# Kernel tuning notes

Hardware: AMD Instinct MI355X
Metric: run time of the kernel (lower is better)

The kernel has to match this reference:

```python
import jax, jax.numpy as jnp
import numpy as np

B, N, IN_DIM, HID, K = 32, 512, 1024, 512, 3
ALPHA = 0.2  # leaky_relu negative slope
NEG = -9e15


def setup_inputs() -> dict:
    key = jax.random.key(0)
    ks = jax.random.split(key, 7)
    hidden_states = jax.random.normal(ks[0], (B, N, IN_DIM), jnp.float32)
    adj = (jax.random.uniform(ks[1], (B, 3, N, N)) < 0.05).astype(jnp.float32)
    W_all = jax.random.normal(ks[2], (3, K, IN_DIM, HID), jnp.float32) * 0.02
    a_all = jax.random.normal(ks[3], (3, K, 2 * HID, 1), jnp.float32) * 0.02
    wawa_w = jax.random.normal(ks[4], (HID, 100), jnp.float32) * 0.05
    wawa_b = jnp.zeros((100,), jnp.float32)
    ctx_w = jax.random.normal(ks[5], (100, 1), jnp.float32) * 0.05
    return {"hidden_states": hidden_states, "adj": adj, "W_all": W_all,
            "a_all": a_all, "wawa_w": wawa_w, "wawa_b": wawa_b, "ctx_w": ctx_w}


def _gat(adj_m, x, W, a):
    # e_ij = leaky_relu(cat[h_i, h_j] @ a) == leaky_relu(h_i@a1 + h_j@a2)
    h = jnp.einsum('bnf,fh->bnh', x, W)           # [B,N,HID]
    f1 = jnp.einsum('bnh,ho->bno', h, a[:HID])    # [B,N,1]
    f2 = jnp.einsum('bnh,ho->bno', h, a[HID:])    # [B,N,1]
    e = jax.nn.leaky_relu(f1 + jnp.swapaxes(f2, 1, 2), negative_slope=ALPHA)  # [B,N,N]
    att = jnp.where(adj_m > 0, e, NEG)
    att = jax.nn.softmax(att, axis=2)
    return jnp.einsum('bnm,bmh->bnh', att, h)


def reference(hidden_states, adj, W_all, a_all, wawa_w, wawa_b, ctx_w):
    adj_a, adj_b, adj_c = adj[:, 0], adj[:, 1], adj[:, 2]
    pa, pb, pc = adj_a, adj_b, adj_c  # matmuls(A, k) = A^(k+1)
    hs = []
    for layer in range(K):
        if layer > 0:
            pa = jnp.matmul(pa, adj_a)
            pb = jnp.matmul(pb, adj_b)
            pc = jnp.matmul(pc, adj_c)
        h_layer = (_gat(pa, hidden_states, W_all[0, layer], a_all[0, layer])
                   + _gat(pb, hidden_states, W_all[1, layer], a_all[1, layer])
                   + _gat(pc, hidden_states, W_all[2, layer], a_all[2, layer]))
        hs.append(h_layer)
    # attention-based combination over the K orders
    s = [jnp.einsum('bnc,co->bno', jnp.tanh(jnp.einsum('bnh,hc->bnc', h, wawa_w) + wawa_b), ctx_w)
         for h in hs]                              # each [B,N,1]
    vs = jax.nn.softmax(jnp.concatenate(s, axis=2), axis=2)  # [B,N,K]
    h_stack = jnp.stack(hs, axis=2)                # [B,N,K,HID]
    return jnp.sum(vs[..., None] * h_stack, axis=2)  # [B,N,HID]
```

## Files before the change

kernel.cpp:

```cpp
#include <hip/hip_runtime.h>
#include <hip/hip_bf16.h>

typedef short v8s __attribute__((ext_vector_type(8)));
typedef float v4f __attribute__((ext_vector_type(4)));
typedef unsigned long long u64;

#define ALPHA 0.2f

__device__ inline unsigned short f32_bf16(float x){
    unsigned int u = __float_as_uint(x);
    unsigned int r = (u + 0x7fffu + ((u >> 16) & 1u)) >> 16;
    return (unsigned short)r;
}
__device__ inline float bf16_f32(unsigned short s){
    return __uint_as_float(((unsigned int)s) << 16);
}
__device__ inline v4f mfma16(v8s a, v8s b, v4f c){
    return __builtin_amdgcn_mfma_f32_16x16x32_bf16(a, b, c, 0, 0, 0);
}
__device__ inline void gload16(const unsigned short* g, short* l){
    __builtin_amdgcn_global_load_lds((const __attribute__((address_space(1))) unsigned int*)g,
                                     (__attribute__((address_space(3))) unsigned int*)l,
                                     16, 0, 0);
}


__global__ void k_convert_x(const float* __restrict__ x, v8s* __restrict__ out, int n8){
    int i = blockIdx.x * 256 + threadIdx.x;
    if (i >= n8) return;
    const float4* p = (const float4*)x + (size_t)i * 2;
    float4 a = p[0], b = p[1];
    v8s r;
    r[0] = (short)f32_bf16(a.x); r[1] = (short)f32_bf16(a.y);
    r[2] = (short)f32_bf16(a.z); r[3] = (short)f32_bf16(a.w);
    r[4] = (short)f32_bf16(b.x); r[5] = (short)f32_bf16(b.y);
    r[6] = (short)f32_bf16(b.z); r[7] = (short)f32_bf16(b.w);
    out[i] = r;
}

__global__ void k_transpose_w(const float* __restrict__ W, unsigned short* __restrict__ Wt){
    __shared__ float tile[32][33];
    int g = blockIdx.z, k0 = blockIdx.x * 32, h0 = blockIdx.y * 32;
    int tx = threadIdx.x, ty = threadIdx.y;
    #pragma unroll
    for (int i = 0; i < 4; ++i)
        tile[ty + i*8][tx] = W[((size_t)g*1024 + k0 + ty + i*8)*512 + h0 + tx];
    __syncthreads();
    #pragma unroll
    for (int i = 0; i < 4; ++i){
        int h = ty + i*8;
        Wt[((size_t)g*512 + h0 + h)*1024 + k0 + tx] = f32_bf16(tile[tx][h]);
    }
}

__global__ void k_wawat(const float* __restrict__ w, unsigned short* __restrict__ wt){
    int i = blockIdx.x * 256 + threadIdx.x;
    if (i >= 128 * 512) return;
    int c = i >> 9, k = i & 511;
    wt[i] = (c < 100) ? f32_bf16(w[k*100 + c]) : (unsigned short)0;
}


__global__ void k_bits(const float* __restrict__ adj, u64* __restrict__ bits){
    int row = blockIdx.x;
    int t = row >> 14, b = (row >> 9) & 31, i = row & 511;
    const float* src = adj + (((size_t)b*3 + t)*512 + i)*512;
    int lane = threadIdx.x;
    #pragma unroll
    for (int w = 0; w < 8; ++w){
        u64 word = __ballot(src[w*64 + lane] > 0.5f);
        if (lane == 0) bits[(size_t)row*8 + w] = word;
    }
}

__global__ __launch_bounds__(256) void k_boolmm(const u64* __restrict__ prev,
                                                const u64* __restrict__ base,
                                                u64* __restrict__ out){
    int row = blockIdx.x * 256 + threadIdx.x;
    if (row >= 49152) return;
    int tb = row >> 9;
    const u64* pr = prev + (size_t)row * 8;
    const u64* bb = base + ((size_t)tb << 9) * 8;
    ulonglong2 a0 = {0,0}, a1 = {0,0}, a2 = {0,0}, a3 = {0,0};
    #pragma unroll
    for (int w = 0; w < 8; ++w){
        u64 m = pr[w];
        const u64* bw = bb + (size_t)(w << 6) * 8;
        while (m){
            int k = __builtin_ctzll(m);
            m &= m - 1;
            const ulonglong2* br = (const ulonglong2*)(bw + (size_t)k * 8);
            ulonglong2 b0 = br[0], b1 = br[1], b2 = br[2], b3 = br[3];
            a0.x |= b0.x; a0.y |= b0.y;
            a1.x |= b1.x; a1.y |= b1.y;
            a2.x |= b2.x; a2.y |= b2.y;
            a3.x |= b3.x; a3.y |= b3.y;
        }
    }
    ulonglong2* op = (ulonglong2*)(out + (size_t)row * 8);
    op[0] = a0; op[1] = a1; op[2] = a2; op[3] = a3;
}

__global__ __launch_bounds__(256, 4) void k_gemm_h(
    const unsigned short* __restrict__ Wt, const unsigned short* __restrict__ Xb,
    unsigned short* __restrict__ Ht, int l)
{
    __shared__ __align__(16) short As[128*32];
    __shared__ __align__(16) short Bs[128*32];
    const int bn = blockIdx.x, bm = blockIdx.y, t = blockIdx.z;
    const int g = t*3 + l;
    const int tid = threadIdx.x;
    const int lane = tid & 63, wave = tid >> 6;
    const int wr = wave >> 1, wc = wave & 1;
    const int fr = lane & 15, fq = lane >> 4;
    const int slot = fq ^ (fr & 3) ^ ((fr >> 2) & 3);

    const int srow = tid >> 2, sw = tid & 3;
    const int gw = sw ^ (srow & 3) ^ ((srow >> 2) & 3);
    const unsigned short* Ap = Wt + ((size_t)g*512 + (size_t)bm*128 + srow)*1024 + gw*8;
    const unsigned short* Bp = Xb + ((size_t)bn*128 + srow)*1024 + gw*8;
    short* AsW = As + wave*512;
    short* BsW = Bs + wave*512;

    v4f acc[4][4] = {};

    for (int kt = 0; kt < 32; ++kt){
        const unsigned short* a0 = Ap + kt*32;
        const unsigned short* b0 = Bp + kt*32;
        gload16(a0,           AsW);
        gload16(a0 + 64*1024, AsW + 2048);
        gload16(b0,           BsW);
        gload16(b0 + 64*1024, BsW + 2048);
        __syncthreads();
        v8s af[4], bf[4];
        #pragma unroll
        for (int i = 0; i < 4; ++i) af[i] = *(const v8s*)&As[(wr*64 + i*16 + fr)*32 + slot*8];
        #pragma unroll
        for (int i = 0; i < 4; ++i) bf[i] = *(const v8s*)&Bs[(wc*64 + i*16 + fr)*32 + slot*8];
        #pragma unroll
        for (int i = 0; i < 4; ++i)
            #pragma unroll
            for (int j = 0; j < 4; ++j)
                acc[i][j] = mfma16(af[i], bf[j], acc[i][j]);
        __syncthreads();
    }
    #pragma unroll
    for (int i = 0; i < 4; ++i){
        const int h = bm*128 + wr*64 + i*16 + fq*4;
        #pragma unroll
        for (int j = 0; j < 4; ++j){
            const int mc = bn*128 + wc*64 + j*16 + fr;
            unsigned short* dst = Ht + ((size_t)t*512 + h)*16384 + mc;
            #pragma unroll
            for (int rg = 0; rg < 4; ++rg)
                dst[(size_t)rg*16384] = f32_bf16(acc[i][j][rg]);
        }
    }
}

__global__ __launch_bounds__(256) void k_f1f2(
    const unsigned short* __restrict__ Ht, const float* __restrict__ aall,
    float* __restrict__ f1, float* __restrict__ f2, int l)
{
    __shared__ float red[256][4];
    const int t = blockIdx.y;
    const int ml = threadIdx.x & 63, hq = threadIdx.x >> 6;
    const int m = (blockIdx.x * 64 + ml) * 2;
    const float* a1 = aall + ((size_t)t*3 + l)*1024;
    const float* a2 = a1 + 512;
    const unsigned int* hp = (const unsigned int*)(Ht + (size_t)t*512*16384 + m);
    float s1a = 0.f, s1b = 0.f, s2a = 0.f, s2b = 0.f;
    #pragma unroll 4
    for (int hh = 0; hh < 128; ++hh){
        int h = hq*128 + hh;
        unsigned int pv = hp[(size_t)h*8192];
        float va = bf16_f32((unsigned short)(pv & 0xffffu));
        float vb = bf16_f32((unsigned short)(pv >> 16));
        float c1 = a1[h], c2 = a2[h];
        s1a += va*c1; s2a += va*c2;
        s1b += vb*c1; s2b += vb*c2;
    }
    red[threadIdx.x][0] = s1a; red[threadIdx.x][1] = s1b;
    red[threadIdx.x][2] = s2a; red[threadIdx.x][3] = s2b;
    __syncthreads();
    if (hq == 0){
        #pragma unroll
        for (int j = 1; j < 4; ++j){
            s1a += red[ml + 64*j][0]; s1b += red[ml + 64*j][1];
            s2a += red[ml + 64*j][2]; s2b += red[ml + 64*j][3];
        }
        f1[t*16384 + m]     = s1a;
        f1[t*16384 + m + 1] = s1b;
        f2[t*16384 + m]     = s2a;
        f2[t*16384 + m + 1] = s2b;
    }
}

__device__ inline void softmax_row(int t, int b, int rt, int r, int q,
    const float* __restrict__ f1a, const float* __restrict__ f2a,
    const u64* __restrict__ maskP, float* p)
{
    const float f1v = f1a[t*16384 + b*512 + rt*64 + r];
    const u64 mw = maskP[(((size_t)t*32 + b)*512 + rt*64 + r)*8 + q];
    const float4* f2p = (const float4*)(f2a + t*16384 + b*512 + q*64);
    float sm = 0.f;
    #pragma unroll
    for (int w = 0; w < 16; ++w){
        float4 f4 = f2p[w];
        #pragma unroll
        for (int u2 = 0; u2 < 4; ++u2){
            int u = w*4 + u2;
            float e = f1v + ((const float*)&f4)[u2];
            e = (e >= 0.f) ? e : ALPHA*e;
            float pe = ((mw >> u) & 1ull) ? __expf(e) : 0.f;
            p[u] = pe; sm += pe;
        }
    }
    sm += __shfl_xor(sm, 1);
    sm += __shfl_xor(sm, 2);
    sm += __shfl_xor(sm, 4);
    const float rinv = 1.f / (sm + 1e-30f);
    #pragma unroll
    for (int u = 0; u < 64; ++u) p[u] *= rinv;
}

__device__ inline void store_att(short* __restrict__ attbuf, int r, int q,
                                 const float* p)
{
    #pragma unroll
    for (int j8 = 0; j8 < 8; ++j8){
        v8s pk;
        #pragma unroll
        for (int u = 0; u < 8; ++u) pk[u] = (short)f32_bf16(p[j8*8 + u]);
        const int cs = q*8 + (j8 ^ q);
        *(v8s*)&attbuf[r*520 + cs*8] = pk;
    }
}

__device__ inline void pv_accum(const short* __restrict__ attbuf,
    const unsigned short* __restrict__ Hb, int wave, int fr, int fq, v4f acc[4][4])
{
    #pragma unroll 2
    for (int kk = 0; kk < 16; ++kk){
        v8s af[4], bv[4];
        const int cb = kk*4 + fq;
        const int cs = (cb & 56) | ((cb & 7) ^ ((cb >> 3) & 7));
        #pragma unroll
        for (int i = 0; i < 4; ++i)
            af[i] = *(const v8s*)&attbuf[(i*16 + fr)*520 + cs*8];
        #pragma unroll
        for (int j = 0; j < 4; ++j)
            bv[j] = *(const v8s*)(Hb + (size_t)(wave*64 + j*16 + fr)*16384 + kk*32 + fq*8);
        #pragma unroll
        for (int i = 0; i < 4; ++i)
            #pragma unroll
            for (int j = 0; j < 4; ++j)
                acc[i][j] = mfma16(af[i], bv[j], acc[i][j]);
    }
}

__global__ __launch_bounds__(512, 2) void k_att_pv(
    const unsigned short* __restrict__ Ht,
    const float* __restrict__ f1a, const float* __restrict__ f2a,
    const u64* __restrict__ maskP,
    unsigned short* __restrict__ hlb)
{
    __shared__ __align__(16) short att0[64*520];
    __shared__ __align__(16) short att1[64*520];
    const int tid = threadIdx.x;
    const int lane = tid & 63, wave = tid >> 6;
    const int b = blockIdx.x, rt = blockIdx.y;
    const int r = tid >> 3, q = tid & 7;
    const int fr = lane & 15, fq = lane >> 4;
    v4f acc[4][4] = {};
    float p[64];

    const unsigned short* Hb0 = Ht + (size_t)b*512;

    softmax_row(0, b, rt, r, q, f1a, f2a, maskP, p);
    store_att(att0, r, q, p);
    __syncthreads();

    softmax_row(1, b, rt, r, q, f1a, f2a, maskP, p);
    store_att(att1, r, q, p);
    pv_accum(att0, Hb0, wave, fr, fq, acc);
    __syncthreads();

    softmax_row(2, b, rt, r, q, f1a, f2a, maskP, p);
    store_att(att0, r, q, p);
    pv_accum(att1, Hb0 + (size_t)512*16384, wave, fr, fq, acc);
    __syncthreads();

    pv_accum(att0, Hb0 + (size_t)2*512*16384, wave, fr, fq, acc);

    #pragma unroll
    for (int i = 0; i < 4; ++i){
        const int row = rt*64 + i*16 + fq*4;
        #pragma unroll
        for (int j = 0; j < 4; ++j){
            const int col = wave*64 + j*16 + fr;
            unsigned short* d1 = hlb + ((size_t)b*512 + row)*512 + col;
            #pragma unroll
            for (int rg = 0; rg < 4; ++rg)
                d1[(size_t)rg*512] = f32_bf16(acc[i][j][rg]);
        }
    }
}

__global__ __launch_bounds__(256) void k_gemm_s(
    const unsigned short* __restrict__ Hb, const unsigned short* __restrict__ Wwt,
    float* __restrict__ C1)
{
    __shared__ __align__(16) short As[128*32];
    __shared__ __align__(16) short Bs[128*32];
    const int bm = blockIdx.x;
    const int tid = threadIdx.x;
    const int lane = tid & 63, wave = tid >> 6;
    const int wr = wave >> 1, wc = wave & 1;
    const int fr = lane & 15, fq = lane >> 4;
    const int slot = fq ^ (fr & 3) ^ ((fr >> 2) & 3);
    const int srow = tid >> 2, sw = tid & 3;
    const int gw = sw ^ (srow & 3) ^ ((srow >> 2) & 3);
    const unsigned short* Ap = Hb + ((size_t)bm*128 + srow)*512 + gw*8;
    const unsigned short* Bp = Wwt + (size_t)srow*512 + gw*8;

    v4f acc[4][4] = {};
    v8s ra0 = *(const v8s*)(Ap);
    v8s ra1 = *(const v8s*)(Ap + 64*512);
    v8s rb0 = *(const v8s*)(Bp);
    v8s rb1 = *(const v8s*)(Bp + 64*512);

    for (int kt = 0; kt < 16; ++kt){
        __syncthreads();
        *(v8s*)&As[tid*8]        = ra0;
        *(v8s*)&As[tid*8 + 2048] = ra1;
        *(v8s*)&Bs[tid*8]        = rb0;
        *(v8s*)&Bs[tid*8 + 2048] = rb1;
        __syncthreads();
        if (kt + 1 < 16){
            const unsigned short* An = Ap + (kt+1)*32;
            const unsigned short* Bn = Bp + (kt+1)*32;
            ra0 = *(const v8s*)(An); ra1 = *(const v8s*)(An + 64*512);
            rb0 = *(const v8s*)(Bn); rb1 = *(const v8s*)(Bn + 64*512);
        }
        v8s af[4], bf[4];
        #pragma unroll
        for (int i = 0; i < 4; ++i) af[i] = *(const v8s*)&As[(wr*64 + i*16 + fr)*32 + slot*8];
        #pragma unroll
        for (int i = 0; i < 4; ++i) bf[i] = *(const v8s*)&Bs[(wc*64 + i*16 + fr)*32 + slot*8];
        #pragma unroll
        for (int i = 0; i < 4; ++i)
            #pragma unroll
            for (int j = 0; j < 4; ++j)
                acc[i][j] = mfma16(af[i], bf[j], acc[i][j]);
    }
    #pragma unroll
    for (int i = 0; i < 4; ++i)
        #pragma unroll
        for (int j = 0; j < 4; ++j)
            #pragma unroll
            for (int rg = 0; rg < 4; ++rg)
                C1[((size_t)bm*128 + wr*64 + i*16 + fq*4 + rg)*128 + wc*64 + j*16 + fr]
                    = acc[i][j][rg];
}

__global__ void k_sv(const float* __restrict__ C1, const float* __restrict__ wb,
                     const float* __restrict__ cw, float* __restrict__ v)
{
    int m = blockIdx.x * 256 + threadIdx.x;
    if (m >= 16384) return;
    float s[3];
    #pragma unroll
    for (int l = 0; l < 3; ++l){
        const float* row = C1 + ((size_t)l*16384 + m)*128;
        float a = 0.f;
        for (int c = 0; c < 100; ++c){
            float x = row[c] + wb[c];
            float th;
            if (x > 15.f) th = 1.f;
            else if (x < -15.f) th = -1.f;
            else { float ex = __expf(2.f*x); th = (ex - 1.f) / (ex + 1.f); }
            a += th * cw[c];
        }
        s[l] = a;
    }
    float m0 = fmaxf(s[0], fmaxf(s[1], s[2]));
    float e0 = __expf(s[0]-m0), e1 = __expf(s[1]-m0), e2 = __expf(s[2]-m0);
    float inv = 1.f / (e0 + e1 + e2);
    v[m] = e0*inv; v[16384 + m] = e1*inv; v[32768 + m] = e2*inv;
}

__global__ void k_comb(const unsigned short* __restrict__ hlb, const float* __restrict__ v,
                       float* __restrict__ out)
{
    int idx = blockIdx.x * 256 + threadIdx.x;
    if (idx >= 16384*64) return;
    int m = idx >> 6, c8 = (idx & 63) << 3;
    const unsigned short* hp = hlb + (size_t)m*512 + c8;
    v8s a = *(const v8s*)hp;
    v8s bb = *(const v8s*)(hp + (size_t)16384*512);
    v8s cc = *(const v8s*)(hp + (size_t)2*16384*512);
    float v0 = v[m], v1 = v[16384+m], v2 = v[32768+m];
    float o[8];
    #pragma unroll
    for (int u = 0; u < 8; ++u)
        o[u] = v0*bf16_f32((unsigned short)a[u])
             + v1*bf16_f32((unsigned short)bb[u])
             + v2*bf16_f32((unsigned short)cc[u]);
    float4* dst = (float4*)(out + (size_t)m*512 + c8);
    dst[0] = make_float4(o[0], o[1], o[2], o[3]);
    dst[1] = make_float4(o[4], o[5], o[6], o[7]);
}

extern "C" void kernel_launch(void* const* d_in, const int* in_sizes, int n_in,
                              void* d_out, int out_size, void* d_ws, size_t ws_size,
                              hipStream_t stream)
{
    (void)in_sizes; (void)n_in; (void)out_size; (void)ws_size;
    const float* hs   = (const float*)d_in[0];
    const float* adj  = (const float*)d_in[1];
    const float* W    = (const float*)d_in[2];
    const float* aall = (const float*)d_in[3];
    const float* ww   = (const float*)d_in[4];
    const float* wb   = (const float*)d_in[5];
    const float* cw   = (const float*)d_in[6];
    float* out = (float*)d_out;
    char* ws = (char*)d_ws;

    unsigned short* Xb  = (unsigned short*)(ws);
    unsigned short* Wt  = (unsigned short*)(ws + 33554432);
    unsigned short* Wwt = (unsigned short*)(ws + 42991616);
    u64* bits           = (u64*)(ws + 43122688);
    u64* P2             = (u64*)(ws + 46268416);
    u64* P3             = (u64*)(ws + 49414144);
    unsigned short* Ht  = (unsigned short*)(ws + 52559872);
    float* f1           = (float*)(ws + 102891520);
    float* f2           = (float*)(ws + 103088128);
    unsigned short* hlb = (unsigned short*)(ws + 203948032);
    float* C1           = (float*)(ws + 52559872);
    float* vv           = (float*)(ws + 102891520);

    k_convert_x<<<8192, 256, 0, stream>>>(hs, (v8s*)Xb, 2097152);
    k_transpose_w<<<dim3(32,16,9), dim3(32,8), 0, stream>>>(W, Wt);
    k_wawat<<<256, 256, 0, stream>>>(ww, Wwt);
    k_bits<<<49152, 64, 0, stream>>>(adj, bits);
    k_boolmm<<<192, 256, 0, stream>>>(bits, bits, P2);
    k_boolmm<<<192, 256, 0, stream>>>(bits, P2, P3);

    const u64* masks[3] = {bits, P2, P3};
    for (int l = 0; l < 3; ++l){
        k_gemm_h<<<dim3(128,4,3), 256, 0, stream>>>(Wt, Xb, Ht, l);
        k_f1f2<<<dim3(128,3), 256, 0, stream>>>(Ht, aall, f1, f2, l);
        k_att_pv<<<dim3(32,8), 512, 0, stream>>>(Ht, f1, f2, masks[l],
            hlb + (size_t)l*16384*512);
    }
    k_gemm_s<<<384, 256, 0, stream>>>(hlb, Wwt, C1);
    k_sv<<<64, 256, 0, stream>>>(C1, wb, cw, vv);
    k_comb<<<4096, 256, 0, stream>>>(hlb, vv, out);
}
```

Before: 624.9 us.

## Fuse f1/f2 projection into GEMM epilogue, batch bit-packing rows, prefetch PV operands

The f1/f2 attention projections are now computed from the fp32 accumulators in the k_gemm_h epilogue. Partial sums go through shuffles and shared memory, then a small k_f1red kernel adds the four bm partials. This removes the k_f1f2 kernel, which re-read the whole bf16 H tensor with strided loads. k_bits now packs four rows per 256-thread block instead of one row per 64-thread block, and pv_accum double-buffers the global H operand loads one k-step ahead. The fused epilogue takes the projection from fp32 accumulators rather than bf16-rounded H, which changes numerics slightly, and the prefetch adds register pressure.

```diff
diff --git a/kernel.cpp b/kernel.cpp
--- a/kernel.cpp
+++ b/kernel.cpp
@@ -61,11 +61,12 @@
 }
 
 
-__global__ void k_bits(const float* __restrict__ adj, u64* __restrict__ bits){
-    int row = blockIdx.x;
+__global__ __launch_bounds__(256) void k_bits(const float* __restrict__ adj,
+                                              u64* __restrict__ bits){
+    int row = blockIdx.x * 4 + (threadIdx.x >> 6);
     int t = row >> 14, b = (row >> 9) & 31, i = row & 511;
     const float* src = adj + (((size_t)b*3 + t)*512 + i)*512;
-    int lane = threadIdx.x;
+    int lane = threadIdx.x & 63;
     #pragma unroll
     for (int w = 0; w < 8; ++w){
         u64 word = __ballot(src[w*64 + lane] > 0.5f);
@@ -103,7 +104,8 @@
 
 __global__ __launch_bounds__(256, 4) void k_gemm_h(
     const unsigned short* __restrict__ Wt, const unsigned short* __restrict__ Xb,
-    unsigned short* __restrict__ Ht, int l)
+    unsigned short* __restrict__ Ht, const float* __restrict__ aall,
+    float* __restrict__ f1p, float* __restrict__ f2p, int l)
 {
     __shared__ __align__(16) short As[128*32];
     __shared__ __align__(16) short Bs[128*32];
@@ -156,44 +158,62 @@
                 dst[(size_t)rg*16384] = f32_bf16(acc[i][j][rg]);
         }
     }
-}
-
-__global__ __launch_bounds__(256) void k_f1f2(
-    const unsigned short* __restrict__ Ht, const float* __restrict__ aall,
-    float* __restrict__ f1, float* __restrict__ f2, int l)
-{
-    __shared__ float red[256][4];
-    const int t = blockIdx.y;
-    const int ml = threadIdx.x & 63, hq = threadIdx.x >> 6;
-    const int m = (blockIdx.x * 64 + ml) * 2;
     const float* a1 = aall + ((size_t)t*3 + l)*1024;
     const float* a2 = a1 + 512;
-    const unsigned int* hp = (const unsigned int*)(Ht + (size_t)t*512*16384 + m);
-    float s1a = 0.f, s1b = 0.f, s2a = 0.f, s2b = 0.f;
-    #pragma unroll 4
-    for (int hh = 0; hh < 128; ++hh){
-        int h = hq*128 + hh;
-        unsigned int pv = hp[(size_t)h*8192];
-        float va = bf16_f32((unsigned short)(pv & 0xffffu));
-        float vb = bf16_f32((unsigned short)(pv >> 16));
-        float c1 = a1[h], c2 = a2[h];
-        s1a += va*c1; s2a += va*c2;
-        s1b += vb*c1; s2b += vb*c2;
-    }
-    red[threadIdx.x][0] = s1a; red[threadIdx.x][1] = s1b;
-    red[threadIdx.x][2] = s2a; red[threadIdx.x][3] = s2b;
+    float s1[4] = {0.f,0.f,0.f,0.f}, s2[4] = {0.f,0.f,0.f,0.f};
+    #pragma unroll
+    for (int i = 0; i < 4; ++i){
+        #pragma unroll
+        for (int rg = 0; rg < 4; ++rg){
+            const int h = bm*128 + wr*64 + i*16 + fq*4 + rg;
+            const float c1 = a1[h], c2 = a2[h];
+            #pragma unroll
+            for (int j = 0; j < 4; ++j){
+                s1[j] += acc[i][j][rg]*c1;
+                s2[j] += acc[i][j][rg]*c2;
+            }
+        }
+    }
+    #pragma unroll
+    for (int j = 0; j < 4; ++j){
+        s1[j] += __shfl_xor(s1[j], 16); s1[j] += __shfl_xor(s1[j], 32);
+        s2[j] += __shfl_xor(s2[j], 16); s2[j] += __shfl_xor(s2[j], 32);
+    }
+    float* scr = (float*)As;
     __syncthreads();
-    if (hq == 0){
-        #pragma unroll
-        for (int j = 1; j < 4; ++j){
-            s1a += red[ml + 64*j][0]; s1b += red[ml + 64*j][1];
-            s2a += red[ml + 64*j][2]; s2b += red[ml + 64*j][3];
-        }
-        f1[t*16384 + m]     = s1a;
-        f1[t*16384 + m + 1] = s1b;
-        f2[t*16384 + m]     = s2a;
-        f2[t*16384 + m + 1] = s2b;
-    }
+    if (fq == 0){
+        #pragma unroll
+        for (int j = 0; j < 4; ++j){
+            scr[(((wr*2 + wc)*4 + j)*16 + fr)*2 + 0] = s1[j];
+            scr[(((wr*2 + wc)*4 + j)*16 + fr)*2 + 1] = s2[j];
+        }
+    }
+    __syncthreads();
+    if (tid < 256){
+        const int which = tid & 1, fr2 = (tid >> 1) & 15, j2 = (tid >> 5) & 3,
+                  wc2 = (tid >> 7) & 1;
+        const float v = scr[(((0*2 + wc2)*4 + j2)*16 + fr2)*2 + which]
+                      + scr[(((1*2 + wc2)*4 + j2)*16 + fr2)*2 + which];
+        const int m = bn*128 + wc2*64 + j2*16 + fr2;
+        float* dst = which ? f2p : f1p;
+        dst[((size_t)bm*3 + t)*16384 + m] = v;
+    }
+}
+
+__global__ __launch_bounds__(256) void k_f1red(
+    const float* __restrict__ f1p, const float* __restrict__ f2p,
+    float* __restrict__ f1, float* __restrict__ f2)
+{
+    int idx = blockIdx.x * 256 + threadIdx.x;
+    if (idx >= 49152) return;
+    float s1 = 0.f, s2 = 0.f;
+    #pragma unroll
+    for (int bm = 0; bm < 4; ++bm){
+        int t = idx >> 14, m = idx & 16383;
+        s1 += f1p[((size_t)bm*3 + t)*16384 + m];
+        s2 += f2p[((size_t)bm*3 + t)*16384 + m];
+    }
+    f1[idx] = s1; f2[idx] = s2;
 }
 
 __device__ inline void softmax_row(int t, int b, int rt, int r, int q,
@@ -240,22 +260,44 @@
 __device__ inline void pv_accum(const short* __restrict__ attbuf,
     const unsigned short* __restrict__ Hb, int wave, int fr, int fq, v4f acc[4][4])
 {
-    #pragma unroll 2
+    v8s bv0[4], bv1[4];
+    #pragma unroll
+    for (int j = 0; j < 4; ++j)
+        bv0[j] = *(const v8s*)(Hb + (size_t)(wave*64 + j*16 + fr)*16384 + fq*8);
+    #pragma unroll
     for (int kk = 0; kk < 16; ++kk){
-        v8s af[4], bv[4];
+        if (kk + 1 < 16){
+            if ((kk + 1) & 1){
+                #pragma unroll
+                for (int j = 0; j < 4; ++j)
+                    bv1[j] = *(const v8s*)(Hb + (size_t)(wave*64 + j*16 + fr)*16384
+                                           + (kk+1)*32 + fq*8);
+            } else {
+                #pragma unroll
+                for (int j = 0; j < 4; ++j)
+                    bv0[j] = *(const v8s*)(Hb + (size_t)(wave*64 + j*16 + fr)*16384
+                                           + (kk+1)*32 + fq*8);
+            }
+        }
+        v8s af[4];
         const int cb = kk*4 + fq;
         const int cs = (cb & 56) | ((cb & 7) ^ ((cb >> 3) & 7));
         #pragma unroll
         for (int i = 0; i < 4; ++i)
             af[i] = *(const v8s*)&attbuf[(i*16 + fr)*520 + cs*8];
-        #pragma unroll
-        for (int j = 0; j < 4; ++j)
-            bv[j] = *(const v8s*)(Hb + (size_t)(wave*64 + j*16 + fr)*16384 + kk*32 + fq*8);
-        #pragma unroll
-        for (int i = 0; i < 4; ++i)
-            #pragma unroll
-            for (int j = 0; j < 4; ++j)
-                acc[i][j] = mfma16(af[i], bv[j], acc[i][j]);
+        if (kk & 1){
+            #pragma unroll
+            for (int i = 0; i < 4; ++i)
+                #pragma unroll
+                for (int j = 0; j < 4; ++j)
+                    acc[i][j] = mfma16(af[i], bv1[j], acc[i][j]);
+        } else {
+            #pragma unroll
+            for (int i = 0; i < 4; ++i)
+                #pragma unroll
+                for (int j = 0; j < 4; ++j)
+                    acc[i][j] = mfma16(af[i], bv0[j], acc[i][j]);
+        }
     }
 }
 
@@ -436,6 +478,8 @@
     unsigned short* Ht  = (unsigned short*)(ws + 52559872);
     float* f1           = (float*)(ws + 102891520);
     float* f2           = (float*)(ws + 103088128);
+    float* f1p          = (float*)(ws + 103284736);
+    float* f2p          = (float*)(ws + 104071168);
     unsigned short* hlb = (unsigned short*)(ws + 203948032);
     float* C1           = (float*)(ws + 52559872);
     float* vv           = (float*)(ws + 102891520);
@@ -443,14 +487,14 @@
     k_convert_x<<<8192, 256, 0, stream>>>(hs, (v8s*)Xb, 2097152);
     k_transpose_w<<<dim3(32,16,9), dim3(32,8), 0, stream>>>(W, Wt);
     k_wawat<<<256, 256, 0, stream>>>(ww, Wwt);
-    k_bits<<<49152, 64, 0, stream>>>(adj, bits);
+    k_bits<<<12288, 256, 0, stream>>>(adj, bits);
     k_boolmm<<<192, 256, 0, stream>>>(bits, bits, P2);
     k_boolmm<<<192, 256, 0, stream>>>(bits, P2, P3);
 
     const u64* masks[3] = {bits, P2, P3};
     for (int l = 0; l < 3; ++l){
-        k_gemm_h<<<dim3(128,4,3), 256, 0, stream>>>(Wt, Xb, Ht, l);
-        k_f1f2<<<dim3(128,3), 256, 0, stream>>>(Ht, aall, f1, f2, l);
+        k_gemm_h<<<dim3(128,4,3), 256, 0, stream>>>(Wt, Xb, Ht, aall, f1p, f2p, l);
+        k_f1red<<<192, 256, 0, stream>>>(f1p, f2p, f1, f2);
         k_att_pv<<<dim3(32,8), 512, 0, stream>>>(Ht, f1, f2, masks[l],
             hlb + (size_t)l*16384*512);
     }
```

New measurement: 592.9 us. 1.05x faster.
